# Optimization experiments

Hardware: AMD Instinct MI355X
Metric: run time of the kernel (lower is better)

Reference implementation:

```python
import jax, jax.numpy as jnp
import numpy as np

B, S, D = 32, 512, 1024
H, HD = 16, 64          # num_heads, head_dim
K = 64                  # downsampling_k
NEG = -9e15             # -9000000000000000.0 in source


def setup_inputs() -> dict:
    key0 = jax.random.key(0)
    ks = jax.random.split(key0, 8)
    glorot = lambda k, shape, fan: jax.random.uniform(k, shape, jnp.float32,
                                                      -np.sqrt(6.0 / fan), np.sqrt(6.0 / fan))
    fan = D + H * HD  # glorot_uniform over (hidden, heads*head_dim)
    return {
        "query": jax.random.normal(ks[0], (B, S, D), jnp.float32),
        "key": jax.random.normal(ks[1], (B, S, D), jnp.float32),
        "value": jax.random.normal(ks[2], (B, S, D), jnp.float32),
        "query_kernel": glorot(ks[3], (D, H, HD), fan),
        "key_kernel": glorot(ks[4], (D, H, HD), fan),
        "value_kernel": glorot(ks[5], (D, H, HD), fan),
        "key_downsample_mat": (1.0 / K) * jax.random.normal(ks[6], (K, S), jnp.float32),
        "value_downsample_mat": (1.0 / K) * jax.random.normal(ks[7], (K, S), jnp.float32),
    }


def reference(query, key, value, query_kernel, key_kernel, value_kernel,
              key_downsample_mat, value_downsample_mat):
    # Linformer-style downsampling of K/V along the sequence axis: [B,S,D] -> [B,K,D]
    key_ds = jnp.einsum('ks,bsd->bkd', key_downsample_mat, key)
    val_ds = jnp.einsum('ks,bsd->bkd', value_downsample_mat, value)

    # Per-head projections
    q = jnp.einsum('bsd,dnh->bsnh', query, query_kernel)   # [B,S,H,HD]
    k = jnp.einsum('bkd,dnh->bknh', key_ds, key_kernel)    # [B,K,H,HD]
    v = jnp.einsum('bkd,dnh->bknh', val_ds, value_kernel)  # [B,K,H,HD]

    # Masked softmax attention over the downsampled key set
    scores = jnp.einsum('bqnh,bknh->bnqk', q, k)           # [B,H,S,K]
    # Source builds tril over [S, K_down] then slices first K cols (no-op here)
    mask = jnp.tril(jnp.ones((S, K), dtype=bool))          # [S,K], broadcasts over B,H
    scores = jnp.where(mask, scores, NEG)
    attn = jax.nn.softmax(scores, axis=-1)                 # dropout deterministic (train=False)

    a_v = jnp.einsum('bnqk,bknh->bqnh', attn, v)           # [B,S,H,HD]
    return a_v.reshape(B, S, H * HD)
```

## Files before the change

kernel.cpp:

```cpp
#include <hip/hip_runtime.h>
#include <stdint.h>

#define B_   32
#define S_   512
#define D_   1024
#define H_   16
#define HD_  64
#define KD_  64
#define NH_  1024

typedef __attribute__((ext_vector_type(8))) short short8;
typedef __attribute__((ext_vector_type(4))) float floatx4;

#define GAS __attribute__((address_space(1)))
#define LAS __attribute__((address_space(3)))

__device__ __forceinline__ ushort f2bf(float f) {
  uint32_t u = __float_as_uint(f);
  u = u + 0x7FFFu + ((u >> 16) & 1u);
  return (ushort)(u >> 16);
}

__device__ __forceinline__ float bf2f(ushort h) {
  return __uint_as_float(((uint32_t)h) << 16);
}

__device__ __forceinline__ void gload_lds16(const void* g, void* l) {
  __builtin_amdgcn_global_load_lds((const GAS uint32_t*)g, (LAS uint32_t*)l, 16, 0, 0);
}

#define BARRIER() asm volatile("s_barrier" ::: "memory")
#define WAITLGKM() asm volatile("s_waitcnt lgkmcnt(0)" ::: "memory")

__global__ __launch_bounds__(256) void cvt_split(const float* __restrict__ kdm,
                                                 const float* __restrict__ vdm,
                                                 ushort* __restrict__ hi,
                                                 ushort* __restrict__ lo) {
  int i = blockIdx.x * 256 + threadIdx.x;
  const float* src = (i < 8192) ? kdm : vdm;
  int j = i & 8191;
  float4 v = ((const float4*)src)[j];
  ushort4 h, l;
  h.x = f2bf(v.x); l.x = f2bf(v.x - bf2f(h.x));
  h.y = f2bf(v.y); l.y = f2bf(v.y - bf2f(h.y));
  h.z = f2bf(v.z); l.z = f2bf(v.z - bf2f(h.z));
  h.w = f2bf(v.w); l.w = f2bf(v.w - bf2f(h.w));
  ((ushort4*)hi)[i] = h;
  ((ushort4*)lo)[i] = l;
}

__global__ __launch_bounds__(256, 6) void pre_kv(
    const float* __restrict__ key, const float* __restrict__ value,
    const float* __restrict__ kkm, const float* __restrict__ vkm,
    const ushort* __restrict__ dsm_hi, const ushort* __restrict__ dsm_lo,
    ushort* __restrict__ kkT, ushort* __restrict__ vkT,
    ushort* __restrict__ outk, ushort* __restrict__ outv) {
  __shared__ __align__(16) char smem[26624];
  const int blk = blockIdx.x;
  const int tid = threadIdx.x;

  if (blk < 512) {
    const int bz = (blk & 7) + ((blk >> 6) << 3);
    const int t  = (blk >> 3) & 7;
    const int z = bz >> 5, b = bz & 31;
    const int c0 = t * 128;
    const float* in = z ? value : key;
    ushort* out     = z ? outv : outk;
    const ushort* Ah = dsm_hi + (size_t)z * (KD_ * S_);
    const ushort* Al = dsm_lo + (size_t)z * (KD_ * S_);

    ushort* lAh = (ushort*)smem;
    ushort* lAl = (ushort*)(smem + 4096);
    uint*   lBh = (uint*)(smem + 8192);
    uint*   lBl = (uint*)(smem + 17408);

    const int lane = tid & 63, w = tid >> 6;
    const int lr = lane & 15, lg = lane >> 4;
    const int wn = w * 32;
    const int lam = tid & 31;
    const int d0 = lam * 4;
    const int sp = tid >> 5;

    floatx4 acc[4][2];
#pragma unroll
    for (int m = 0; m < 4; ++m)
#pragma unroll
      for (int n = 0; n < 2; ++n) acc[m][n] = (floatx4){0.f, 0.f, 0.f, 0.f};

    for (int k0 = 0; k0 < S_; k0 += 32) {
      {
        size_t src = (size_t)(tid >> 2) * S_ + k0 + (size_t)(tid & 3) * 8;
        gload_lds16(Ah + src, lAh + w * 512);
        gload_lds16(Al + src, lAl + w * 512);
      }
      float4 ra[2], rb[2];
#pragma unroll
      for (int si = 0; si < 2; ++si) {
        int s = sp * 2 + si * 16;
        const float* p = in + ((size_t)(b * S_ + k0 + s)) * D_ + c0 + d0;
        ra[si] = *(const float4*)p;
        rb[si] = *(const float4*)(p + D_);
      }
      const int swz = lam & 12;
#pragma unroll
      for (int si = 0; si < 2; ++si) {
        int col = (sp + si * 8) ^ swz;
        const float* pa = (const float*)&ra[si];
        const float* pb = (const float*)&rb[si];
#pragma unroll
        for (int i = 0; i < 4; ++i) {
          ushort h0 = f2bf(pa[i]);
          ushort l0 = f2bf(pa[i] - bf2f(h0));
          ushort h1 = f2bf(pb[i]);
          ushort l1 = f2bf(pb[i] - bf2f(h1));
          lBh[(d0 + i) * 18 + col] = (uint)h0 | ((uint)h1 << 16);
          lBl[(d0 + i) * 18 + col] = (uint)l0 | ((uint)l1 << 16);
        }
      }
      __syncthreads();
      short8 bh[2], bl[2];
#pragma unroll
      for (int n = 0; n < 2; ++n) {
        int d = wn + n * 16 + lr;
        int off = d * 18 + ((lg * 4) ^ ((d >> 2) & 12));
        bh[n] = *(const short8*)&lBh[off];
        bl[n] = *(const short8*)&lBl[off];
      }
#pragma unroll
      for (int m = 0; m < 4; ++m) {
        int aoff = (m * 16 + lr) * 32 + lg * 8;
        short8 ah = *(const short8*)&lAh[aoff];
        short8 al = *(const short8*)&lAl[aoff];
#pragma unroll
        for (int n = 0; n < 2; ++n) {
          acc[m][n] = __builtin_amdgcn_mfma_f32_16x16x32_bf16(ah, bh[n], acc[m][n], 0, 0, 0);
          acc[m][n] = __builtin_amdgcn_mfma_f32_16x16x32_bf16(ah, bl[n], acc[m][n], 0, 0, 0);
          acc[m][n] = __builtin_amdgcn_mfma_f32_16x16x32_bf16(al, bh[n], acc[m][n], 0, 0, 0);
        }
      }
      __syncthreads();
    }
    size_t obase = (size_t)b * KD_ * D_;
#pragma unroll
    for (int m = 0; m < 4; ++m)
#pragma unroll
      for (int n = 0; n < 2; ++n)
#pragma unroll
        for (int r = 0; r < 4; ++r)
          out[obase + (size_t)(m * 16 + lg * 4 + r) * D_ + c0 + wn + n * 16 + lr] =
              f2bf(acc[m][n][r]);

  } else {
    const int blk2 = blk - 512;
    const int tz = blk2 >> 10;
    const int rem = blk2 & 1023;
    const int tyb = rem >> 5;
    const int txb = rem & 31;
    const float* in = tz == 0 ? kkm : vkm;
    ushort* outp    = tz == 0 ? kkT : vkT;
    float (*tile)[33] = (float(*)[33])smem;
    const int tx = tid & 31, ty = tid >> 5;
    int x = txb * 32 + tx;
    int y0 = tyb * 32;
#pragma unroll
    for (int j = 0; j < 4; ++j)
      tile[ty + j * 8][tx] = in[(size_t)(y0 + ty + j * 8) * 1024 + x];
    __syncthreads();
    int x2 = tyb * 32 + tx;
    int y2 = txb * 32;
#pragma unroll
    for (int j = 0; j < 4; ++j)
      outp[(size_t)(y2 + ty + j * 8) * 1024 + x2] = f2bf(tile[tx][ty + j * 8]);
  }
}

__global__ __launch_bounds__(256) void gemm_kv_q(
    const ushort* __restrict__ A,
    const ushort* __restrict__ Bt,
    const ushort* __restrict__ Bt2,
    ushort* __restrict__ C,
    const float* __restrict__ qk, ushort* __restrict__ qkT,
    const float* __restrict__ query, ushort* __restrict__ q_bf) {
  __shared__ __align__(16) char smem[16384];
  const int blk = blockIdx.x;
  const int tid = threadIdx.x;

  if (blk < 256) {
    ushort* lA = (ushort*)smem;
    ushort* lB = (ushort*)(smem + 8192);
    int xcd = blk & 7, slot = blk >> 3;
    int mt = xcd * 4 + (slot >> 3);
    int nt = slot & 7;
    int m0 = mt * 128, n0 = nt * 128;
    const ushort* Bsel = (mt >= 16) ? Bt2 : Bt;

    int lane = tid & 63, w = tid >> 6;
    int lr = lane & 15, lg = lane >> 4;
    int wm = (w >> 1) * 64, wn = (w & 1) * 64;
    floatx4 acc[4][4];
#pragma unroll
    for (int m = 0; m < 4; ++m)
#pragma unroll
      for (int n = 0; n < 4; ++n) acc[m][n] = (floatx4){0.f, 0.f, 0.f, 0.f};

    for (int k0 = 0; k0 < 1024; k0 += 32) {
#pragma unroll
      for (int i = 0; i < 2; ++i) {
        int c = i * 256 + w * 64 + lane;
        gload_lds16(A + ((size_t)(m0 + (c >> 2)) * 1024 + k0 + (c & 3) * 8),
                    &lA[(i * 256 + w * 64) * 8]);
        gload_lds16(Bsel + ((size_t)(n0 + (c >> 2)) * 1024 + k0 + (c & 3) * 8),
                    &lB[(i * 256 + w * 64) * 8]);
      }
      __syncthreads();
      short8 af[4], bfr[4];
#pragma unroll
      for (int m = 0; m < 4; ++m)
        af[m] = *(const short8*)&lA[(wm + m * 16 + lr) * 32 + lg * 8];
#pragma unroll
      for (int n = 0; n < 4; ++n)
        bfr[n] = *(const short8*)&lB[(wn + n * 16 + lr) * 32 + lg * 8];
#pragma unroll
      for (int m = 0; m < 4; ++m)
#pragma unroll
        for (int n = 0; n < 4; ++n)
          acc[m][n] = __builtin_amdgcn_mfma_f32_16x16x32_bf16(af[m], bfr[n], acc[m][n], 0, 0, 0);
      __syncthreads();
    }
#pragma unroll
    for (int m = 0; m < 4; ++m)
#pragma unroll
      for (int n = 0; n < 4; ++n)
#pragma unroll
        for (int r = 0; r < 4; ++r)
          C[(size_t)(m0 + wm + m * 16 + lg * 4 + r) * 1024 + n0 + wn + n * 16 + lr] =
              f2bf(acc[m][n][r]);

  } else if (blk < 256 + 1024) {
    const int blk2 = blk - 256;
    const int tyb = blk2 >> 5;
    const int txb = blk2 & 31;
    float (*tile)[33] = (float(*)[33])smem;
    const int tx = tid & 31, ty = tid >> 5;
    int x = txb * 32 + tx;
    int y0 = tyb * 32;
#pragma unroll
    for (int j = 0; j < 4; ++j)
      tile[ty + j * 8][tx] = qk[(size_t)(y0 + ty + j * 8) * 1024 + x];
    __syncthreads();
    int x2 = tyb * 32 + tx;
    int y2 = txb * 32;
#pragma unroll
    for (int j = 0; j < 4; ++j)
      qkT[(size_t)(y2 + ty + j * 8) * 1024 + x2] = f2bf(tile[tx][ty + j * 8]);

  } else {
    const size_t base = (size_t)(blk - 1280) * 2048 + tid;
#pragma unroll
    for (int j = 0; j < 8; ++j) {
      size_t i = base + (size_t)j * 256;
      float4 v = ((const float4*)query)[i];
      ushort4 o;
      o.x = f2bf(v.x); o.y = f2bf(v.y); o.z = f2bf(v.z); o.w = f2bf(v.w);
      ((ushort4*)q_bf)[i] = o;
    }
  }
}

__global__ __launch_bounds__(512, 2) void gemm256_attn(
    const ushort* __restrict__ A, const ushort* __restrict__ Bt,
    const ushort* __restrict__ kp, const ushort* __restrict__ vp,
    float* __restrict__ out) {
  extern __shared__ ushort lds[];
  ushort* ldsA = lds;
  ushort* ldsB = lds + 2 * 256 * 64;
  const int tid = threadIdx.x;
  const int w = tid >> 6, lane = tid & 63;
  const int lr = lane & 15, lg = lane >> 4;
  const int wm = w >> 2, wn = w & 3;
  const int bid = blockIdx.x;
  const int mt = (bid & 7) * 8 + ((bid >> 3) >> 2);
  const int nt = (bid >> 3) & 3;
  const int m0 = mt * 256, n0 = nt * 256;
  const int NT = 16;

  const int srow = tid >> 3;
  const int sslot = tid & 7;

  auto stageA = [&](int sl, int ch, int k0) {
    int rloc = ch * 64 + srow;
    int gs = sslot ^ (rloc & 7);
    gload_lds16(A + (size_t)(m0 + rloc) * 1024 + k0 + gs * 8,
                ldsA + sl * (256 * 64) + ch * (64 * 64) + w * 512);
  };
  auto stageB = [&](int sl, int ch, int k0) {
    int rloc = ch * 64 + srow;
    int gs = sslot ^ (rloc & 7);
    gload_lds16(Bt + (size_t)(n0 + rloc) * 1024 + k0 + gs * 8,
                ldsB + sl * (256 * 64) + ch * (64 * 64) + w * 512);
  };

  short8 af[4][2], bf[2][2];
  auto loadA = [&](int sl, int mh) {
#pragma unroll
    for (int i = 0; i < 4; ++i) {
      int row = wm * 128 + (mh * 4 + i) * 16 + lr;
#pragma unroll
      for (int kk = 0; kk < 2; ++kk) {
        int col = (((kk * 4 + lg) ^ (row & 7)) * 8);
        af[i][kk] = *(const short8*)&ldsA[sl * (256 * 64) + row * 64 + col];
      }
    }
  };
  auto loadB = [&](int sl, int nh) {
#pragma unroll
    for (int j = 0; j < 2; ++j) {
      int row = wn * 64 + (nh * 2 + j) * 16 + lr;
#pragma unroll
      for (int kk = 0; kk < 2; ++kk) {
        int col = (((kk * 4 + lg) ^ (row & 7)) * 8);
        bf[j][kk] = *(const short8*)&ldsB[sl * (256 * 64) + row * 64 + col];
      }
    }
  };

  floatx4 acc[8][4];
#pragma unroll
  for (int i = 0; i < 8; ++i)
#pragma unroll
    for (int j = 0; j < 4; ++j) acc[i][j] = (floatx4){0.f, 0.f, 0.f, 0.f};

  auto mma16 = [&](int mh, int nh) {
    __builtin_amdgcn_s_setprio(1);
#pragma unroll
    for (int i = 0; i < 4; ++i)
#pragma unroll
      for (int j = 0; j < 2; ++j)
#pragma unroll
        for (int kk = 0; kk < 2; ++kk)
          acc[mh * 4 + i][nh * 2 + j] = __builtin_amdgcn_mfma_f32_16x16x32_bf16(
              af[i][kk], bf[j][kk], acc[mh * 4 + i][nh * 2 + j], 0, 0, 0);
    __builtin_amdgcn_s_setprio(0);
  };

#pragma unroll
  for (int ch = 0; ch < 4; ++ch) { stageA(0, ch, 0); stageB(0, ch, 0); }

#pragma unroll 2
  for (int t = 0; t < NT; ++t) {
    const int s = t & 1, ns = s ^ 1;
    const int kn = (t + 1) << 6;
    const bool more = (t + 1 < NT);
    if (more) {
#pragma unroll
      for (int ch = 0; ch < 4; ++ch) { stageA(ns, ch, kn); stageB(ns, ch, kn); }
      asm volatile("s_waitcnt vmcnt(8)" ::: "memory");
    } else {
      asm volatile("s_waitcnt vmcnt(0)" ::: "memory");
    }
    BARRIER();
    loadA(s, 0); loadB(s, 0);
    WAITLGKM();
    mma16(0, 0);
    BARRIER();
    loadB(s, 1);
    BARRIER();
    WAITLGKM();
    mma16(0, 1);
    BARRIER();
    loadA(s, 1);
    BARRIER();
    WAITLGKM();
    mma16(1, 1);
    BARRIER();
    loadB(s, 0);
    BARRIER();
    WAITLGKM();
    mma16(1, 0);
    BARRIER();
  }

  ushort* QP = lds + w * 4608;
  ushort* sV = lds + 8 * 4608;
  const int b = mt >> 1;
  const int hq = nt * 4 + wn;

  {
    int hh = tid >> 7, t2 = tid & 127;
    int k = t2 >> 1, h0 = (t2 & 1) * 32;
    const ushort* src = vp + ((size_t)b * KD_ + k) * 1024 + (nt * 4 + hh) * HD_ + h0;
#pragma unroll
    for (int i = 0; i < 32; ++i) sV[hh * 4608 + (h0 + i) * 72 + k] = src[i];
  }
  __syncthreads();

#pragma unroll
  for (int half = 0; half < 2; ++half) {
    const int srow0 = (mt & 1) * 256 + wm * 128 + half * 64;
#pragma unroll
    for (int mi = 0; mi < 4; ++mi)
#pragma unroll
      for (int nj = 0; nj < 4; ++nj)
#pragma unroll
        for (int r = 0; r < 4; ++r)
          QP[(mi * 16 + lg * 4 + r) * 72 + nj * 16 + lr] =
              f2bf(acc[half * 4 + mi][nj][r]);
    WAITLGKM();
    __builtin_amdgcn_sched_barrier(0);
    floatx4 qacc[4][4];
#pragma unroll
    for (int m = 0; m < 4; ++m)
#pragma unroll
      for (int n = 0; n < 4; ++n) qacc[m][n] = (floatx4){0.f, 0.f, 0.f, 0.f};
#pragma unroll
    for (int kk = 0; kk < 2; ++kk) {
      short8 qa[4], kb[4];
#pragma unroll
      for (int m = 0; m < 4; ++m)
        qa[m] = *(const short8*)&QP[(m * 16 + lr) * 72 + kk * 32 + lg * 8];
#pragma unroll
      for (int n = 0; n < 4; ++n)
        kb[n] = *(const short8*)(kp + ((size_t)b * KD_ + n * 16 + lr) * 1024 +
                                 hq * HD_ + kk * 32 + lg * 8);
#pragma unroll
      for (int m = 0; m < 4; ++m)
#pragma unroll
        for (int n = 0; n < 4; ++n)
          qacc[m][n] = __builtin_amdgcn_mfma_f32_16x16x32_bf16(qa[m], kb[n], qacc[m][n], 0, 0, 0);
    }
#pragma unroll
    for (int m = 0; m < 4; ++m) {
#pragma unroll
      for (int r = 0; r < 4; ++r) {
        int srow2 = srow0 + m * 16 + lg * 4 + r;
        float vals[4];
        float mx = -1e30f;
#pragma unroll
        for (int n = 0; n < 4; ++n) {
          int col = n * 16 + lr;
          float val = qacc[m][n][r];
          val = (col <= srow2) ? val : -1e30f;
          vals[n] = val;
          mx = fmaxf(mx, val);
        }
        mx = fmaxf(mx, __shfl_xor(mx, 1));
        mx = fmaxf(mx, __shfl_xor(mx, 2));
        mx = fmaxf(mx, __shfl_xor(mx, 4));
        mx = fmaxf(mx, __shfl_xor(mx, 8));
        float sum = 0.f;
#pragma unroll
        for (int n = 0; n < 4; ++n) {
          float e = __expf(vals[n] - mx);
          vals[n] = e;
          sum += e;
        }
        sum += __shfl_xor(sum, 1);
        sum += __shfl_xor(sum, 2);
        sum += __shfl_xor(sum, 4);
        sum += __shfl_xor(sum, 8);
        float inv = 1.0f / sum;
#pragma unroll
        for (int n = 0; n < 4; ++n)
          QP[(m * 16 + lg * 4 + r) * 72 + n * 16 + lr] = f2bf(vals[n] * inv);
      }
    }
    WAITLGKM();
    __builtin_amdgcn_sched_barrier(0);
    floatx4 oacc[4][4];
#pragma unroll
    for (int m = 0; m < 4; ++m)
#pragma unroll
      for (int n = 0; n < 4; ++n) oacc[m][n] = (floatx4){0.f, 0.f, 0.f, 0.f};
#pragma unroll
    for (int kk = 0; kk < 2; ++kk) {
      short8 pa[4], vb[4];
#pragma unroll
      for (int m = 0; m < 4; ++m)
        pa[m] = *(const short8*)&QP[(m * 16 + lr) * 72 + kk * 32 + lg * 8];
#pragma unroll
      for (int n = 0; n < 4; ++n)
        vb[n] = *(const short8*)&sV[wn * 4608 + (n * 16 + lr) * 72 + kk * 32 + lg * 8];
#pragma unroll
      for (int m = 0; m < 4; ++m)
#pragma unroll
        for (int n = 0; n < 4; ++n)
          oacc[m][n] = __builtin_amdgcn_mfma_f32_16x16x32_bf16(pa[m], vb[n], oacc[m][n], 0, 0, 0);
    }
#pragma unroll
    for (int m = 0; m < 4; ++m)
#pragma unroll
      for (int n = 0; n < 4; ++n)
#pragma unroll
        for (int r = 0; r < 4; ++r)
          out[((size_t)b * S_ + srow0 + m * 16 + lg * 4 + r) * 1024 +
              hq * HD_ + n * 16 + lr] = oacc[m][n][r];
  }
}

extern "C" void kernel_launch(void* const* d_in, const int* in_sizes, int n_in,
                              void* d_out, int out_size, void* d_ws, size_t ws_size,
                              hipStream_t stream) {
  const float* query = (const float*)d_in[0];
  const float* key   = (const float*)d_in[1];
  const float* value = (const float*)d_in[2];
  const float* qk    = (const float*)d_in[3];
  const float* kk    = (const float*)d_in[4];
  const float* vk    = (const float*)d_in[5];
  const float* kdm   = (const float*)d_in[6];
  const float* vdm   = (const float*)d_in[7];
  float* out = (float*)d_out;

  char* ws = (char*)d_ws;
  if (ws_size < (90ull << 20)) return;
  ushort* q_bf   = (ushort*)(ws);
  ushort* qkT    = (ushort*)(ws + (33ull << 20));
  ushort* kkT    = (ushort*)(ws + (35ull << 20));
  ushort* vkT    = (ushort*)(ws + (37ull << 20));
  ushort* kds    = (ushort*)(ws + (39ull << 20));
  ushort* vds    = (ushort*)(ws + (43ull << 20));
  ushort* k_proj = (ushort*)(ws + (79ull << 20));
  ushort* v_proj = (ushort*)(ws + (83ull << 20));
  ushort* dsm_hi = (ushort*)(ws + (87ull << 20));
  ushort* dsm_lo = (ushort*)(ws + (87ull << 20) + (128ull << 10));

  hipFuncSetAttribute((const void*)gemm256_attn,
                      hipFuncAttributeMaxDynamicSharedMemorySize, 131072);

  cvt_split<<<64, 256, 0, stream>>>(kdm, vdm, dsm_hi, dsm_lo);
  pre_kv<<<512 + 2048, 256, 0, stream>>>(
      key, value, kk, vk, dsm_hi, dsm_lo, kkT, vkT, kds, vds);
  gemm_kv_q<<<256 + 1024 + 2048, 256, 0, stream>>>(
      kds, kkT, vkT, k_proj, qk, qkT, query, q_bf);
  gemm256_attn<<<256, 512, 131072, stream>>>(q_bf, qkT, k_proj, v_proj, out);
}
```

Measured before the change: 131.0 us.

## Use 16 waves per block in fused Q-proj attention kernel, pre-transpose V projection

The fused Q-projection plus attention kernel now runs with 1024 threads (16 waves) per 256x256 tile. Each wave holds a 64x64 accumulator, so the two-half attention epilogue loop is gone. The global-to-LDS staging is interleaved between the MFMA phases instead of issued all at once. The V projection is written out already transposed by the preceding GEMM, so the attention stage reads V fragments straight from global memory instead of building a transposed copy in LDS. This aims for more latency hiding and less epilogue work, at the cost of fewer registers per thread and more global reads of V per wave.

```diff
diff --git a/kernel.cpp b/kernel.cpp
--- a/kernel.cpp
+++ b/kernel.cpp
@@ -179,6 +179,7 @@
     const ushort* __restrict__ Bt,
     const ushort* __restrict__ Bt2,
     ushort* __restrict__ C,
+    ushort* __restrict__ vpT,
     const float* __restrict__ qk, ushort* __restrict__ qkT,
     const float* __restrict__ query, ushort* __restrict__ q_bf) {
   __shared__ __align__(16) char smem[16384];
@@ -227,14 +228,29 @@
           acc[m][n] = __builtin_amdgcn_mfma_f32_16x16x32_bf16(af[m], bfr[n], acc[m][n], 0, 0, 0);
       __syncthreads();
     }
-#pragma unroll
-    for (int m = 0; m < 4; ++m)
-#pragma unroll
-      for (int n = 0; n < 4; ++n)
-#pragma unroll
-        for (int r = 0; r < 4; ++r)
-          C[(size_t)(m0 + wm + m * 16 + lg * 4 + r) * 1024 + n0 + wn + n * 16 + lr] =
-              f2bf(acc[m][n][r]);
+    if (mt < 16) {
+#pragma unroll
+      for (int m = 0; m < 4; ++m)
+#pragma unroll
+        for (int n = 0; n < 4; ++n)
+#pragma unroll
+          for (int r = 0; r < 4; ++r)
+            C[(size_t)(m0 + wm + m * 16 + lg * 4 + r) * 1024 + n0 + wn + n * 16 + lr] =
+                f2bf(acc[m][n][r]);
+    } else {
+#pragma unroll
+      for (int m = 0; m < 4; ++m)
+#pragma unroll
+        for (int n = 0; n < 4; ++n) {
+          int rowV = m0 - 2048 + wm + m * 16 + lg * 4;
+          int b = rowV >> 6, k = rowV & 63;
+          int hd = n0 + wn + n * 16 + lr;
+          ushort4 o;
+          o.x = f2bf(acc[m][n][0]); o.y = f2bf(acc[m][n][1]);
+          o.z = f2bf(acc[m][n][2]); o.w = f2bf(acc[m][n][3]);
+          *(ushort4*)&vpT[(size_t)b * 65536 + (size_t)hd * 64 + k] = o;
+        }
+    }
 
   } else if (blk < 256 + 1024) {
     const int blk2 = blk - 256;
@@ -267,9 +283,9 @@
   }
 }
 
-__global__ __launch_bounds__(512, 2) void gemm256_attn(
+__global__ __launch_bounds__(1024) void gemm256_attn(
     const ushort* __restrict__ A, const ushort* __restrict__ Bt,
-    const ushort* __restrict__ kp, const ushort* __restrict__ vp,
+    const ushort* __restrict__ kp, const ushort* __restrict__ vpT,
     float* __restrict__ out) {
   extern __shared__ ushort lds[];
   ushort* ldsA = lds;
@@ -288,23 +304,23 @@
   const int sslot = tid & 7;
 
   auto stageA = [&](int sl, int ch, int k0) {
-    int rloc = ch * 64 + srow;
+    int rloc = ch * 128 + srow;
     int gs = sslot ^ (rloc & 7);
     gload_lds16(A + (size_t)(m0 + rloc) * 1024 + k0 + gs * 8,
-                ldsA + sl * (256 * 64) + ch * (64 * 64) + w * 512);
+                ldsA + sl * (256 * 64) + ch * (128 * 64) + w * 512);
   };
   auto stageB = [&](int sl, int ch, int k0) {
-    int rloc = ch * 64 + srow;
+    int rloc = ch * 128 + srow;
     int gs = sslot ^ (rloc & 7);
     gload_lds16(Bt + (size_t)(n0 + rloc) * 1024 + k0 + gs * 8,
-                ldsB + sl * (256 * 64) + ch * (64 * 64) + w * 512);
+                ldsB + sl * (256 * 64) + ch * (128 * 64) + w * 512);
   };
 
-  short8 af[4][2], bf[2][2];
+  short8 af[2][2], bf[2][2];
   auto loadA = [&](int sl, int mh) {
 #pragma unroll
-    for (int i = 0; i < 4; ++i) {
-      int row = wm * 128 + (mh * 4 + i) * 16 + lr;
+    for (int i = 0; i < 2; ++i) {
+      int row = wm * 64 + (mh * 2 + i) * 16 + lr;
 #pragma unroll
       for (int kk = 0; kk < 2; ++kk) {
         int col = (((kk * 4 + lg) ^ (row & 7)) * 8);
@@ -324,177 +340,172 @@
     }
   };
 
-  floatx4 acc[8][4];
-#pragma unroll
-  for (int i = 0; i < 8; ++i)
+  floatx4 acc[4][4];
+#pragma unroll
+  for (int i = 0; i < 4; ++i)
 #pragma unroll
     for (int j = 0; j < 4; ++j) acc[i][j] = (floatx4){0.f, 0.f, 0.f, 0.f};
 
-  auto mma16 = [&](int mh, int nh) {
+  auto mma8 = [&](int mh, int nh) {
     __builtin_amdgcn_s_setprio(1);
 #pragma unroll
-    for (int i = 0; i < 4; ++i)
+    for (int i = 0; i < 2; ++i)
 #pragma unroll
       for (int j = 0; j < 2; ++j)
 #pragma unroll
         for (int kk = 0; kk < 2; ++kk)
-          acc[mh * 4 + i][nh * 2 + j] = __builtin_amdgcn_mfma_f32_16x16x32_bf16(
-              af[i][kk], bf[j][kk], acc[mh * 4 + i][nh * 2 + j], 0, 0, 0);
+          acc[mh * 2 + i][nh * 2 + j] = __builtin_amdgcn_mfma_f32_16x16x32_bf16(
+              af[i][kk], bf[j][kk], acc[mh * 2 + i][nh * 2 + j], 0, 0, 0);
     __builtin_amdgcn_s_setprio(0);
   };
 
-#pragma unroll
-  for (int ch = 0; ch < 4; ++ch) { stageA(0, ch, 0); stageB(0, ch, 0); }
+  stageA(0, 0, 0); stageA(0, 1, 0); stageB(0, 0, 0); stageB(0, 1, 0);
 
 #pragma unroll 2
   for (int t = 0; t < NT; ++t) {
     const int s = t & 1, ns = s ^ 1;
     const int kn = (t + 1) << 6;
     const bool more = (t + 1 < NT);
-    if (more) {
-#pragma unroll
-      for (int ch = 0; ch < 4; ++ch) { stageA(ns, ch, kn); stageB(ns, ch, kn); }
-      asm volatile("s_waitcnt vmcnt(8)" ::: "memory");
-    } else {
-      asm volatile("s_waitcnt vmcnt(0)" ::: "memory");
-    }
+    if (more) { stageA(ns, 0, kn); asm volatile("s_waitcnt vmcnt(1)" ::: "memory"); }
+    else      { asm volatile("s_waitcnt vmcnt(0)" ::: "memory"); }
     BARRIER();
     loadA(s, 0); loadB(s, 0);
     WAITLGKM();
-    mma16(0, 0);
-    BARRIER();
+    mma8(0, 0);
+    BARRIER();
+    if (more) stageA(ns, 1, kn);
     loadB(s, 1);
     BARRIER();
     WAITLGKM();
-    mma16(0, 1);
-    BARRIER();
+    mma8(0, 1);
+    BARRIER();
+    if (more) stageB(ns, 0, kn);
     loadA(s, 1);
     BARRIER();
     WAITLGKM();
-    mma16(1, 1);
-    BARRIER();
+    mma8(1, 1);
+    BARRIER();
+    if (more) stageB(ns, 1, kn);
     loadB(s, 0);
     BARRIER();
     WAITLGKM();
-    mma16(1, 0);
+    mma8(1, 0);
     BARRIER();
   }
 
-  ushort* QP = lds + w * 4608;
-  ushort* sV = lds + 8 * 4608;
+  ushort* QP = lds + w * 4096;
   const int b = mt >> 1;
   const int hq = nt * 4 + wn;
-
-  {
-    int hh = tid >> 7, t2 = tid & 127;
-    int k = t2 >> 1, h0 = (t2 & 1) * 32;
-    const ushort* src = vp + ((size_t)b * KD_ + k) * 1024 + (nt * 4 + hh) * HD_ + h0;
-#pragma unroll
-    for (int i = 0; i < 32; ++i) sV[hh * 4608 + (h0 + i) * 72 + k] = src[i];
+  const int srow0 = (mt & 1) * 256 + wm * 64;
+
+#pragma unroll
+  for (int mi = 0; mi < 4; ++mi)
+#pragma unroll
+    for (int nj = 0; nj < 4; ++nj)
+#pragma unroll
+      for (int r = 0; r < 4; ++r) {
+        int row = mi * 16 + lg * 4 + r, col = nj * 16 + lr;
+        QP[row * 64 + ((((col >> 3) ^ (row & 7)) << 3) | (col & 7))] =
+            f2bf(acc[mi][nj][r]);
+      }
+  WAITLGKM();
+  __builtin_amdgcn_sched_barrier(0);
+  floatx4 qacc[4][4];
+#pragma unroll
+  for (int m = 0; m < 4; ++m)
+#pragma unroll
+    for (int n = 0; n < 4; ++n) qacc[m][n] = (floatx4){0.f, 0.f, 0.f, 0.f};
+#pragma unroll
+  for (int kk = 0; kk < 2; ++kk) {
+    short8 qa[4], kb[4];
+#pragma unroll
+    for (int m = 0; m < 4; ++m) {
+      int row = m * 16 + lr;
+      qa[m] = *(const short8*)&QP[row * 64 + (((kk * 4 + lg) ^ (row & 7)) << 3)];
+    }
+#pragma unroll
+    for (int n = 0; n < 4; ++n)
+      kb[n] = *(const short8*)(kp + ((size_t)b * KD_ + n * 16 + lr) * 1024 +
+                               hq * HD_ + kk * 32 + lg * 8);
+#pragma unroll
+    for (int m = 0; m < 4; ++m)
+#pragma unroll
+      for (int n = 0; n < 4; ++n)
+        qacc[m][n] = __builtin_amdgcn_mfma_f32_16x16x32_bf16(qa[m], kb[n], qacc[m][n], 0, 0, 0);
   }
-  __syncthreads();
-
-#pragma unroll
-  for (int half = 0; half < 2; ++half) {
-    const int srow0 = (mt & 1) * 256 + wm * 128 + half * 64;
-#pragma unroll
-    for (int mi = 0; mi < 4; ++mi)
-#pragma unroll
-      for (int nj = 0; nj < 4; ++nj)
-#pragma unroll
-        for (int r = 0; r < 4; ++r)
-          QP[(mi * 16 + lg * 4 + r) * 72 + nj * 16 + lr] =
-              f2bf(acc[half * 4 + mi][nj][r]);
-    WAITLGKM();
-    __builtin_amdgcn_sched_barrier(0);
-    floatx4 qacc[4][4];
+#pragma unroll
+  for (int m = 0; m < 4; ++m) {
+#pragma unroll
+    for (int r = 0; r < 4; ++r) {
+      int srow2 = srow0 + m * 16 + lg * 4 + r;
+      float vals[4];
+      float mx = -1e30f;
+#pragma unroll
+      for (int n = 0; n < 4; ++n) {
+        int col = n * 16 + lr;
+        float val = qacc[m][n][r];
+        val = (col <= srow2) ? val : -1e30f;
+        vals[n] = val;
+        mx = fmaxf(mx, val);
+      }
+      mx = fmaxf(mx, __shfl_xor(mx, 1));
+      mx = fmaxf(mx, __shfl_xor(mx, 2));
+      mx = fmaxf(mx, __shfl_xor(mx, 4));
+      mx = fmaxf(mx, __shfl_xor(mx, 8));
+      float sum = 0.f;
+#pragma unroll
+      for (int n = 0; n < 4; ++n) {
+        float e = __expf(vals[n] - mx);
+        vals[n] = e;
+        sum += e;
+      }
+      sum += __shfl_xor(sum, 1);
+      sum += __shfl_xor(sum, 2);
+      sum += __shfl_xor(sum, 4);
+      sum += __shfl_xor(sum, 8);
+      float inv = 1.0f / sum;
+#pragma unroll
+      for (int n = 0; n < 4; ++n) {
+        int row = m * 16 + lg * 4 + r, col = n * 16 + lr;
+        QP[row * 64 + ((((col >> 3) ^ (row & 7)) << 3) | (col & 7))] =
+            f2bf(vals[n] * inv);
+      }
+    }
+  }
+  WAITLGKM();
+  __builtin_amdgcn_sched_barrier(0);
+  floatx4 oacc[4][4];
+#pragma unroll
+  for (int m = 0; m < 4; ++m)
+#pragma unroll
+    for (int n = 0; n < 4; ++n) oacc[m][n] = (floatx4){0.f, 0.f, 0.f, 0.f};
+#pragma unroll
+  for (int kk = 0; kk < 2; ++kk) {
+    short8 pa[4], vb[4];
+#pragma unroll
+    for (int m = 0; m < 4; ++m) {
+      int row = m * 16 + lr;
+      pa[m] = *(const short8*)&QP[row * 64 + (((kk * 4 + lg) ^ (row & 7)) << 3)];
+    }
+#pragma unroll
+    for (int n = 0; n < 4; ++n)
+      vb[n] = *(const short8*)(vpT + (size_t)b * 65536 +
+                               (size_t)(hq * HD_ + n * 16 + lr) * 64 +
+                               kk * 32 + lg * 8);
 #pragma unroll
     for (int m = 0; m < 4; ++m)
 #pragma unroll
-      for (int n = 0; n < 4; ++n) qacc[m][n] = (floatx4){0.f, 0.f, 0.f, 0.f};
-#pragma unroll
-    for (int kk = 0; kk < 2; ++kk) {
-      short8 qa[4], kb[4];
-#pragma unroll
-      for (int m = 0; m < 4; ++m)
-        qa[m] = *(const short8*)&QP[(m * 16 + lr) * 72 + kk * 32 + lg * 8];
-#pragma unroll
       for (int n = 0; n < 4; ++n)
-        kb[n] = *(const short8*)(kp + ((size_t)b * KD_ + n * 16 + lr) * 1024 +
-                                 hq * HD_ + kk * 32 + lg * 8);
-#pragma unroll
-      for (int m = 0; m < 4; ++m)
-#pragma unroll
-        for (int n = 0; n < 4; ++n)
-          qacc[m][n] = __builtin_amdgcn_mfma_f32_16x16x32_bf16(qa[m], kb[n], qacc[m][n], 0, 0, 0);
-    }
-#pragma unroll
-    for (int m = 0; m < 4; ++m) {
-#pragma unroll
-      for (int r = 0; r < 4; ++r) {
-        int srow2 = srow0 + m * 16 + lg * 4 + r;
-        float vals[4];
-        float mx = -1e30f;
-#pragma unroll
-        for (int n = 0; n < 4; ++n) {
-          int col = n * 16 + lr;
-          float val = qacc[m][n][r];
-          val = (col <= srow2) ? val : -1e30f;
-          vals[n] = val;
-          mx = fmaxf(mx, val);
-        }
-        mx = fmaxf(mx, __shfl_xor(mx, 1));
-        mx = fmaxf(mx, __shfl_xor(mx, 2));
-        mx = fmaxf(mx, __shfl_xor(mx, 4));
-        mx = fmaxf(mx, __shfl_xor(mx, 8));
-        float sum = 0.f;
-#pragma unroll
-        for (int n = 0; n < 4; ++n) {
-          float e = __expf(vals[n] - mx);
-          vals[n] = e;
-          sum += e;
-        }
-        sum += __shfl_xor(sum, 1);
-        sum += __shfl_xor(sum, 2);
-        sum += __shfl_xor(sum, 4);
-        sum += __shfl_xor(sum, 8);
-        float inv = 1.0f / sum;
-#pragma unroll
-        for (int n = 0; n < 4; ++n)
-          QP[(m * 16 + lg * 4 + r) * 72 + n * 16 + lr] = f2bf(vals[n] * inv);
-      }
-    }
-    WAITLGKM();
-    __builtin_amdgcn_sched_barrier(0);
-    floatx4 oacc[4][4];
-#pragma unroll
-    for (int m = 0; m < 4; ++m)
-#pragma unroll
-      for (int n = 0; n < 4; ++n) oacc[m][n] = (floatx4){0.f, 0.f, 0.f, 0.f};
-#pragma unroll
-    for (int kk = 0; kk < 2; ++kk) {
-      short8 pa[4], vb[4];
-#pragma unroll
-      for (int m = 0; m < 4; ++m)
-        pa[m] = *(const short8*)&QP[(m * 16 + lr) * 72 + kk * 32 + lg * 8];
-#pragma unroll
-      for (int n = 0; n < 4; ++n)
-        vb[n] = *(const short8*)&sV[wn * 4608 + (n * 16 + lr) * 72 + kk * 32 + lg * 8];
-#pragma unroll
-      for (int m = 0; m < 4; ++m)
-#pragma unroll
-        for (int n = 0; n < 4; ++n)
-          oacc[m][n] = __builtin_amdgcn_mfma_f32_16x16x32_bf16(pa[m], vb[n], oacc[m][n], 0, 0, 0);
-    }
-#pragma unroll
-    for (int m = 0; m < 4; ++m)
-#pragma unroll
-      for (int n = 0; n < 4; ++n)
-#pragma unroll
-        for (int r = 0; r < 4; ++r)
-          out[((size_t)b * S_ + srow0 + m * 16 + lg * 4 + r) * 1024 +
-              hq * HD_ + n * 16 + lr] = oacc[m][n][r];
+        oacc[m][n] = __builtin_amdgcn_mfma_f32_16x16x32_bf16(pa[m], vb[n], oacc[m][n], 0, 0, 0);
   }
+#pragma unroll
+  for (int m = 0; m < 4; ++m)
+#pragma unroll
+    for (int n = 0; n < 4; ++n)
+#pragma unroll
+      for (int r = 0; r < 4; ++r)
+        out[((size_t)b * S_ + srow0 + m * 16 + lg * 4 + r) * 1024 +
+            hq * HD_ + n * 16 + lr] = oacc[m][n][r];
 }
 
 extern "C" void kernel_launch(void* const* d_in, const int* in_sizes, int n_in,
@@ -519,7 +530,7 @@
   ushort* kds    = (ushort*)(ws + (39ull << 20));
   ushort* vds    = (ushort*)(ws + (43ull << 20));
   ushort* k_proj = (ushort*)(ws + (79ull << 20));
-  ushort* v_proj = (ushort*)(ws + (83ull << 20));
+  ushort* v_projT= (ushort*)(ws + (83ull << 20));
   ushort* dsm_hi = (ushort*)(ws + (87ull << 20));
   ushort* dsm_lo = (ushort*)(ws + (87ull << 20) + (128ull << 10));
 
@@ -530,6 +541,6 @@
   pre_kv<<<512 + 2048, 256, 0, stream>>>(
       key, value, kk, vk, dsm_hi, dsm_lo, kkT, vkT, kds, vds);
   gemm_kv_q<<<256 + 1024 + 2048, 256, 0, stream>>>(
-      kds, kkT, vkT, k_proj, qk, qkT, query, q_bf);
-  gemm256_attn<<<256, 512, 131072, stream>>>(q_bf, qkT, k_proj, v_proj, out);
-}
+      kds, kkT, vkT, k_proj, v_projT, qk, qkT, query, q_bf);
+  gemm256_attn<<<256, 1024, 131072, stream>>>(q_bf, qkT, k_proj, v_projT, out);
+}
```

Result: slower. 152.6 us (+16.5%).
